# Kernel optimization log

Measured on AMD Instinct MI355X. Metric: run time of the kernel, lower is better.

## Reference

```python
import jax, jax.numpy as jnp
import numpy as np

B, C, W, H = 4, 64, 64, 64
CQK = C // 8  # query/key channels


def setup_inputs() -> dict:
    key = jax.random.key(0)
    ks = jax.random.split(key, 8)
    s = 0.05
    return {
        "x": jax.random.normal(ks[0], (B, C, W, H), jnp.float32),
        "Wq": jax.random.normal(ks[1], (CQK, C), jnp.float32) * s,
        "bq": jax.random.normal(ks[2], (CQK,), jnp.float32) * s,
        "Wk": jax.random.normal(ks[3], (CQK, C), jnp.float32) * s,
        "bk": jax.random.normal(ks[4], (CQK,), jnp.float32) * s,
        "Wv": jax.random.normal(ks[5], (C, C), jnp.float32) * s,
        "bv": jax.random.normal(ks[6], (C,), jnp.float32) * s,
        # torch init is zeros; use a nonzero value so the attention path is exercised
        "gamma": jax.random.normal(ks[7], (1,), jnp.float32) * s,
    }


def reference(x, Wq, bq, Wk, bk, Wv, bv, gamma):
    b, c, w, h = x.shape
    n = w * h
    xf = x.reshape(b, c, n)  # B, C, N
    # 1x1 convs == per-pixel linear maps
    q = jnp.einsum("oc,bcn->bno", Wq, xf) + bq           # B, N, Cqk
    k = jnp.einsum("oc,bcn->bon", Wk, xf) + bk[:, None]   # B, Cqk, N
    energy = jnp.einsum("bno,bom->bnm", q, k)             # B, N, N
    attn = jax.nn.softmax(energy, axis=-1)                # B, N, N
    v = jnp.einsum("oc,bcn->bon", Wv, xf) + bv[:, None]   # B, C, N
    # out[b,c,j] = sum_n v[b,c,n] * attn[j,n]  (bmm with attention^T)
    out = jnp.einsum("bcn,bjn->bcj", v, attn)
    out = out.reshape(b, c, w, h)
    return gamma * out + x
```

## Files before the change

### kernel.cpp

```cpp
#include <hip/hip_runtime.h>

typedef short s16x8 __attribute__((ext_vector_type(8)));
typedef float f32x4 __attribute__((ext_vector_type(4)));
typedef float f32x16 __attribute__((ext_vector_type(16)));
typedef unsigned u32x4 __attribute__((ext_vector_type(4)));

#define BB 4
#define NN 4096
#define LOG2E 1.4426950408889634f

__device__ __forceinline__ unsigned short f2bf(float f) {
    unsigned int u = __builtin_bit_cast(unsigned int, f);
    u += 0x7fff + ((u >> 16) & 1);
    return (unsigned short)(u >> 16);
}

__device__ __forceinline__ unsigned pk2(float lo, float hi) {
    return __builtin_amdgcn_perm(__builtin_bit_cast(unsigned, hi),
                                 __builtin_bit_cast(unsigned, lo), 0x07060302u);
}

__device__ __forceinline__ void gload16(const void* g, void* l) {
    __builtin_amdgcn_global_load_lds(
        (const __attribute__((address_space(1))) unsigned int*)g,
        (__attribute__((address_space(3))) unsigned int*)l, 16, 0, 0);
}

__device__ __forceinline__ void pl32swap(unsigned &a, unsigned &b) {
    asm volatile("v_permlane32_swap_b32 %0, %1" : "+v"(a), "+v"(b));
}

__global__ __launch_bounds__(256) void proj_kernel(
    const float* __restrict__ x,
    const float* __restrict__ Wq, const float* __restrict__ bq,
    const float* __restrict__ Wk, const float* __restrict__ bk,
    const float* __restrict__ Wv, const float* __restrict__ bv,
    unsigned short* __restrict__ Qw, unsigned short* __restrict__ Kw,
    unsigned short* __restrict__ Vw)
{
    __shared__ __attribute__((aligned(16))) unsigned short sW[80 * 72];
    __shared__ __attribute__((aligned(16))) unsigned short xT[64 * 72];
    __shared__ float sb[80];

    int tid = threadIdx.x;
    int b  = blockIdx.x >> 6;
    int n0 = (blockIdx.x & 63) << 6;

    for (int i = tid; i < 1280; i += 256) {
        int o = i >> 4, c4 = (i & 15) << 2;
        const float* src = (o < 8) ? &Wq[o * 64 + c4]
                         : ((o < 16) ? &Wk[(o - 8) * 64 + c4]
                                     : &Wv[(o - 16) * 64 + c4]);
        float4 v = *(const float4*)src;
        float sc = (o < 8) ? LOG2E : 1.f;
        sW[o * 72 + c4 + 0] = f2bf(v.x * sc);
        sW[o * 72 + c4 + 1] = f2bf(v.y * sc);
        sW[o * 72 + c4 + 2] = f2bf(v.z * sc);
        sW[o * 72 + c4 + 3] = f2bf(v.w * sc);
    }
    if (tid < 80)
        sb[tid] = (tid < 8) ? bq[tid] * LOG2E
                            : ((tid < 16) ? bk[tid - 8] : bv[tid - 16]);
    for (int i = tid; i < 1024; i += 256) {
        int c = i >> 4, p4 = (i & 15) << 2;
        float4 v = *(const float4*)&x[(((size_t)b * 64 + c) << 12) + n0 + p4];
        xT[(p4 + 0) * 72 + c] = f2bf(v.x);
        xT[(p4 + 1) * 72 + c] = f2bf(v.y);
        xT[(p4 + 2) * 72 + c] = f2bf(v.z);
        xT[(p4 + 3) * 72 + c] = f2bf(v.w);
    }
    __syncthreads();

    int w = tid >> 6, l = tid & 63, g = l >> 4, q16 = l & 15;
    int pix = w * 16 + q16;

    s16x8 bf0 = *(const s16x8*)&xT[pix * 72 + g * 8];
    s16x8 bf1 = *(const s16x8*)&xT[pix * 72 + 32 + g * 8];

    s16x8 a0[5], a1[5];
#pragma unroll
    for (int ot = 0; ot < 5; ++ot) {
        a0[ot] = *(const s16x8*)&sW[(ot * 16 + q16) * 72 + g * 8];
        a1[ot] = *(const s16x8*)&sW[(ot * 16 + q16) * 72 + 32 + g * 8];
    }
    __syncthreads();

    unsigned short* sV = xT;
    size_t base16 = ((size_t)(b << 12) + n0 + pix) << 4;

#pragma unroll
    for (int ot = 0; ot < 5; ++ot) {
        f32x4 acc = {0.f, 0.f, 0.f, 0.f};
        acc = __builtin_amdgcn_mfma_f32_16x16x32_bf16(a0[ot], bf0, acc, 0, 0, 0);
        acc = __builtin_amdgcn_mfma_f32_16x16x32_bf16(a1[ot], bf1, acc, 0, 0, 0);
#pragma unroll
        for (int r = 0; r < 4; ++r) {
            int orow = ot * 16 + g * 4 + r;
            unsigned short hv = f2bf(acc[r] + sb[orow]);
            if (ot == 0) {
                if (orow < 8) {
                    Qw[base16 + orow] = hv;
                    Qw[base16 + orow + 8] = 0;
                } else {
                    Kw[base16 + orow - 8] = hv;
                    Kw[base16 + orow] = 0;
                }
            } else {
                sV[(orow - 16) * 72 + pix] = hv;
            }
        }
    }
    __syncthreads();

#pragma unroll
    for (int i = tid; i < 512; i += 256) {
        int c = i >> 3, oct = i & 7;
        u32x4 v = *(const u32x4*)&sV[c * 72 + oct * 8];
        *(u32x4*)&Vw[(((size_t)b * 64 + c) << 12) + n0 + oct * 8] = v;
    }
}

__global__ __launch_bounds__(1024, 4) void attn_kernel(
    const unsigned short* __restrict__ Qw, const unsigned short* __restrict__ Kw,
    const unsigned short* __restrict__ Vw, const float* __restrict__ x,
    const float* __restrict__ gamma, float* __restrict__ out)
{
    __shared__ __attribute__((aligned(16))) char smem[150784];
    const int OOFF = 131072, LOFF = 148480, GLOFF = 150528;

    int tid = threadIdx.x;
    int w = tid >> 6, l = tid & 63, r31 = l & 31, hi = l >> 5;
    int wq = w >> 3, wk = w & 7;
    int b  = blockIdx.x >> 6;
    int n0 = (blockIdx.x & 63) << 6;
    float gm = gamma[0];

    const char* vsrc = (const char*)Vw + ((size_t)b << 19) + ((size_t)w << 13)
                     + ((l ^ (w & 7)) << 4);
    char* vdst = smem + w * 1024;

    const char* Qb = (const char*)Qw + ((size_t)b << 17);
    s16x8 qf = *(const s16x8*)(Qb + ((size_t)(n0 + wq * 32 + r31) << 5) + (hi << 4));
    const char* Kb = (const char*)Kw + ((size_t)b << 17)
                   + ((size_t)r31 << 5) + (hi << 4);

    f32x16 acc0, acc1;
#pragma unroll
    for (int i = 0; i < 16; ++i) { acc0[i] = 0.f; acc1[i] = 0.f; }
    float la = 0.f;

    gload16(vsrc, vdst);
    gload16(vsrc + (16 << 13), vdst + 16 * 1024);
    gload16(vsrc + (32 << 13), vdst + 32 * 1024);
    gload16(vsrc + (48 << 13), vdst + 48 * 1024);
    __syncthreads();

    for (int t = 0; t < 8; ++t) {
        int buf = t & 1;
        if (t < 7) {
            int bo = (buf ^ 1) << 16;
            const char* vs = vsrc + (size_t)(t + 1) * 1024;
            gload16(vs,             vdst + bo);
            gload16(vs + (16 << 13), vdst + bo + 16 * 1024);
            gload16(vs + (32 << 13), vdst + bo + 32 * 1024);
            gload16(vs + (48 << 13), vdst + bo + 48 * 1024);
        }
        const char* Vt = smem + (buf << 16);

        int kk0 = (t << 9) + (wk << 6);
        s16x8 kfA = *(const s16x8*)(Kb + ((size_t)kk0 << 5));
        s16x8 kfB = *(const s16x8*)(Kb + ((size_t)(kk0 + 32) << 5));

#pragma unroll
        for (int ci = 0; ci < 2; ++ci) {
            s16x8 kf = ci ? kfB : kfA;

            f32x16 E;
            {
                f32x16 z;
#pragma unroll
                for (int i = 0; i < 16; ++i) z[i] = 0.f;
                E = __builtin_amdgcn_mfma_f32_32x32x16_bf16(kf, qf, z, 0, 0, 0);
            }
#pragma unroll
            for (int i = 0; i < 16; ++i) E[i] = __builtin_amdgcn_exp2f(E[i]);
            la += (((E[0] + E[1]) + (E[2] + E[3])) + ((E[4] + E[5]) + (E[6] + E[7])))
                + (((E[8] + E[9]) + (E[10] + E[11])) + ((E[12] + E[13]) + (E[14] + E[15])));

            unsigned x0 = pk2(E[0], E[1]),  x1 = pk2(E[2], E[3]);
            unsigned x2 = pk2(E[4], E[5]),  x3 = pk2(E[6], E[7]);
            unsigned x4 = pk2(E[8], E[9]),  x5 = pk2(E[10], E[11]);
            unsigned x6 = pk2(E[12], E[13]), x7 = pk2(E[14], E[15]);
            pl32swap(x0, x2); pl32swap(x1, x3);
            pl32swap(x4, x6); pl32swap(x5, x7);
            u32x4 u0 = {x0, x1, x2, x3}, u1 = {x4, x5, x6, x7};
            s16x8 pf0 = __builtin_bit_cast(s16x8, u0);
            s16x8 pf1 = __builtin_bit_cast(s16x8, u1);

            int jb = (wk << 3) + (ci << 2);
            int sj0 = (((jb + hi) ^ (r31 & 7)) << 4);
            int sj1 = (((jb + 2 + hi) ^ (r31 & 7)) << 4);
            const char* row_lo = Vt + (r31 << 10);
            const char* row_hi = row_lo + (32 << 10);
            s16x8 vA0 = *(const s16x8*)(row_lo + sj0);
            s16x8 vA1 = *(const s16x8*)(row_lo + sj1);
            s16x8 vB0 = *(const s16x8*)(row_hi + sj0);
            s16x8 vB1 = *(const s16x8*)(row_hi + sj1);

            acc0 = __builtin_amdgcn_mfma_f32_32x32x16_bf16(vA0, pf0, acc0, 0, 0, 0);
            acc0 = __builtin_amdgcn_mfma_f32_32x32x16_bf16(vA1, pf1, acc0, 0, 0, 0);
            acc1 = __builtin_amdgcn_mfma_f32_32x32x16_bf16(vB0, pf0, acc1, 0, 0, 0);
            acc1 = __builtin_amdgcn_mfma_f32_32x32x16_bf16(vB1, pf1, acc1, 0, 0, 0);
        }
        __syncthreads();
    }

    la += __shfl_xor(la, 32);
    float* sL = (float*)(smem + LOFF);
    if (l < 32) sL[wk * 64 + wq * 32 + l] = la;

    float* sO = (float*)(smem + OOFF);
#pragma unroll
    for (int s = 0; s < 8; ++s) {
#pragma unroll
        for (int B = 0; B < 8; ++B) {
            if (((wk + s) & 7) == B) {
                const int R2 = B & 3;
                float e0 = (B < 4) ? acc0[R2 * 4 + 0] : acc1[R2 * 4 + 0];
                float e1 = (B < 4) ? acc0[R2 * 4 + 1] : acc1[R2 * 4 + 1];
                float e2 = (B < 4) ? acc0[R2 * 4 + 2] : acc1[R2 * 4 + 2];
                float e3 = (B < 4) ? acc0[R2 * 4 + 3] : acc1[R2 * 4 + 3];
                float* p = &sO[(B * 8 + hi * 4) * 68 + wq * 32 + r31];
                if (s == 0) {
                    p[0] = e0; p[68] = e1; p[136] = e2; p[204] = e3;
                } else {
                    p[0] += e0; p[68] += e1; p[136] += e2; p[204] += e3;
                }
            }
        }
        __syncthreads();
    }

    float* sGL = (float*)(smem + GLOFF);
    if (tid < 64) {
        float L = 0.f;
#pragma unroll
        for (int wk2 = 0; wk2 < 8; ++wk2) L += sL[wk2 * 64 + tid];
        sGL[tid] = gm / L;
    }
    __syncthreads();

#pragma unroll
    for (int pp = 0; pp < 4; ++pp) {
        int c = pp * 16 + w;
        size_t idx = (((size_t)b * 64 + c) << 12) + n0 + l;
        out[idx] = sGL[l] * sO[c * 68 + l] + x[idx];
    }
}

extern "C" void kernel_launch(void* const* d_in, const int* in_sizes, int n_in,
                              void* d_out, int out_size, void* d_ws, size_t ws_size,
                              hipStream_t stream) {
    const float* x     = (const float*)d_in[0];
    const float* Wq    = (const float*)d_in[1];
    const float* bq    = (const float*)d_in[2];
    const float* Wk    = (const float*)d_in[3];
    const float* bk    = (const float*)d_in[4];
    const float* Wv    = (const float*)d_in[5];
    const float* bv    = (const float*)d_in[6];
    const float* gamma = (const float*)d_in[7];
    float* out = (float*)d_out;

    unsigned short* Qw = (unsigned short*)d_ws;
    unsigned short* Kw = Qw + (size_t)BB * NN * 16;
    unsigned short* Vw = Kw + (size_t)BB * NN * 16;

    proj_kernel<<<256, 256, 0, stream>>>(x, Wq, bq, Wk, bk, Wv, bv, Qw, Kw, Vw);
    attn_kernel<<<256, 1024, 0, stream>>>(Qw, Kw, Vw, x, gamma, out);
}
```

Before: 31.51 us.

## Split attention into 512 blocks of 32 queries with 8 key-split waves

The attention kernel moves from 256 blocks of 1024 threads (64 queries, 2x8 waves) to 512 blocks of 512 threads (32 queries, 8 key-split waves). The halved shared-memory footprint allows two blocks per CU, and the K/V streaming loop now runs 16 smaller double-buffered steps, prefetching K fragments and waiting with vmcnt plus a raw barrier instead of a full syncthreads. The epilogue writes output with float4 vectorized stores. In exchange, V tiles are loaded twice as often across blocks and more barriers are executed per block.

Measured after the change: 34.82 us. +10.5%, slower.

```diff
diff --git a/kernel.cpp b/kernel.cpp
--- a/kernel.cpp
+++ b/kernel.cpp
@@ -120,141 +120,142 @@
     }
 }
 
-__global__ __launch_bounds__(1024, 4) void attn_kernel(
+__global__ __launch_bounds__(512, 2) void attn_kernel(
     const unsigned short* __restrict__ Qw, const unsigned short* __restrict__ Kw,
     const unsigned short* __restrict__ Vw, const float* __restrict__ x,
     const float* __restrict__ gamma, float* __restrict__ out)
 {
-    __shared__ __attribute__((aligned(16))) char smem[150784];
-    const int OOFF = 131072, LOFF = 148480, GLOFF = 150528;
+    __shared__ __attribute__((aligned(16))) char smem[75904];
+    const int OOFF = 65536, LOFF = 74752, GLOFF = 75776;
 
     int tid = threadIdx.x;
     int w = tid >> 6, l = tid & 63, r31 = l & 31, hi = l >> 5;
-    int wq = w >> 3, wk = w & 7;
-    int b  = blockIdx.x >> 6;
-    int n0 = (blockIdx.x & 63) << 6;
+    int b  = blockIdx.x >> 7;
+    int n0 = (blockIdx.x & 127) << 5;
     float gm = gamma[0];
 
-    const char* vsrc = (const char*)Vw + ((size_t)b << 19) + ((size_t)w << 13)
-                     + ((l ^ (w & 7)) << 4);
-    char* vdst = smem + w * 1024;
-
-    const char* Qb = (const char*)Qw + ((size_t)b << 17);
-    s16x8 qf = *(const s16x8*)(Qb + ((size_t)(n0 + wq * 32 + r31) << 5) + (hi << 4));
-    const char* Kb = (const char*)Kw + ((size_t)b << 17)
-                   + ((size_t)r31 << 5) + (hi << 4);
-
-    f32x16 acc0, acc1;
-#pragma unroll
-    for (int i = 0; i < 16; ++i) { acc0[i] = 0.f; acc1[i] = 0.f; }
+    const char* Vb = (const char*)Vw + ((size_t)b << 19);
+    const char* vs0, *vs1, *vs2, *vs3;
+    {
+        int rr = (w << 3) + hi;
+        vs0 = Vb + ((size_t)(rr + 0) << 13) + (((r31) ^ (0 + hi)) << 4);
+        vs1 = Vb + ((size_t)(rr + 2) << 13) + (((r31) ^ (2 + hi)) << 4);
+        vs2 = Vb + ((size_t)(rr + 4) << 13) + (((r31) ^ (4 + hi)) << 4);
+        vs3 = Vb + ((size_t)(rr + 6) << 13) + (((r31) ^ (6 + hi)) << 4);
+    }
+    char* vd = smem + (w << 12);
+
+    s16x8 qf = *(const s16x8*)((const char*)Qw + ((size_t)b << 17)
+                               + ((size_t)(n0 + r31) << 5) + (hi << 4));
+    const char* Kbw = (const char*)Kw + ((size_t)b << 17) + (w << 10)
+                    + ((size_t)r31 << 5) + (hi << 4);
+
+    f32x16 acc0, acc1, zz;
+#pragma unroll
+    for (int i = 0; i < 16; ++i) { acc0[i] = 0.f; acc1[i] = 0.f; zz[i] = 0.f; }
     float la = 0.f;
 
-    gload16(vsrc, vdst);
-    gload16(vsrc + (16 << 13), vdst + 16 * 1024);
-    gload16(vsrc + (32 << 13), vdst + 32 * 1024);
-    gload16(vsrc + (48 << 13), vdst + 48 * 1024);
-    __syncthreads();
-
-    for (int t = 0; t < 8; ++t) {
-        int buf = t & 1;
-        if (t < 7) {
-            int bo = (buf ^ 1) << 16;
-            const char* vs = vsrc + (size_t)(t + 1) * 1024;
-            gload16(vs,             vdst + bo);
-            gload16(vs + (16 << 13), vdst + bo + 16 * 1024);
-            gload16(vs + (32 << 13), vdst + bo + 32 * 1024);
-            gload16(vs + (48 << 13), vdst + bo + 48 * 1024);
-        }
-        const char* Vt = smem + (buf << 16);
-
-        int kk0 = (t << 9) + (wk << 6);
-        s16x8 kfA = *(const s16x8*)(Kb + ((size_t)kk0 << 5));
-        s16x8 kfB = *(const s16x8*)(Kb + ((size_t)(kk0 + 32) << 5));
-
-#pragma unroll
-        for (int ci = 0; ci < 2; ++ci) {
-            s16x8 kf = ci ? kfB : kfA;
-
-            f32x16 E;
-            {
-                f32x16 z;
-#pragma unroll
-                for (int i = 0; i < 16; ++i) z[i] = 0.f;
-                E = __builtin_amdgcn_mfma_f32_32x32x16_bf16(kf, qf, z, 0, 0, 0);
-            }
-#pragma unroll
-            for (int i = 0; i < 16; ++i) E[i] = __builtin_amdgcn_exp2f(E[i]);
-            la += (((E[0] + E[1]) + (E[2] + E[3])) + ((E[4] + E[5]) + (E[6] + E[7])))
-                + (((E[8] + E[9]) + (E[10] + E[11])) + ((E[12] + E[13]) + (E[14] + E[15])));
-
-            unsigned x0 = pk2(E[0], E[1]),  x1 = pk2(E[2], E[3]);
-            unsigned x2 = pk2(E[4], E[5]),  x3 = pk2(E[6], E[7]);
-            unsigned x4 = pk2(E[8], E[9]),  x5 = pk2(E[10], E[11]);
-            unsigned x6 = pk2(E[12], E[13]), x7 = pk2(E[14], E[15]);
-            pl32swap(x0, x2); pl32swap(x1, x3);
-            pl32swap(x4, x6); pl32swap(x5, x7);
-            u32x4 u0 = {x0, x1, x2, x3}, u1 = {x4, x5, x6, x7};
-            s16x8 pf0 = __builtin_bit_cast(s16x8, u0);
-            s16x8 pf1 = __builtin_bit_cast(s16x8, u1);
-
-            int jb = (wk << 3) + (ci << 2);
-            int sj0 = (((jb + hi) ^ (r31 & 7)) << 4);
-            int sj1 = (((jb + 2 + hi) ^ (r31 & 7)) << 4);
-            const char* row_lo = Vt + (r31 << 10);
-            const char* row_hi = row_lo + (32 << 10);
-            s16x8 vA0 = *(const s16x8*)(row_lo + sj0);
-            s16x8 vA1 = *(const s16x8*)(row_lo + sj1);
-            s16x8 vB0 = *(const s16x8*)(row_hi + sj0);
-            s16x8 vB1 = *(const s16x8*)(row_hi + sj1);
-
-            acc0 = __builtin_amdgcn_mfma_f32_32x32x16_bf16(vA0, pf0, acc0, 0, 0, 0);
-            acc0 = __builtin_amdgcn_mfma_f32_32x32x16_bf16(vA1, pf1, acc0, 0, 0, 0);
-            acc1 = __builtin_amdgcn_mfma_f32_32x32x16_bf16(vB0, pf0, acc1, 0, 0, 0);
-            acc1 = __builtin_amdgcn_mfma_f32_32x32x16_bf16(vB1, pf1, acc1, 0, 0, 0);
-        }
-        __syncthreads();
+    gload16(vs0, vd); gload16(vs1, vd + 1024);
+    gload16(vs2, vd + 2048); gload16(vs3, vd + 3072);
+    s16x8 kf_next = *(const s16x8*)(Kbw);
+    asm volatile("s_waitcnt vmcnt(1)" ::: "memory");
+    __builtin_amdgcn_s_barrier();
+
+    for (int t = 0; t < 16; ++t) {
+        s16x8 kf = kf_next;
+        const char* Vt = smem + ((t & 1) << 15);
+        if (t < 15) {
+            int bo = (((t & 1) ^ 1) << 15);
+            char* d = vd + bo;
+            size_t so = (size_t)(t + 1) << 9;
+            gload16(vs0 + so, d);        gload16(vs1 + so, d + 1024);
+            gload16(vs2 + so, d + 2048); gload16(vs3 + so, d + 3072);
+            kf_next = *(const s16x8*)(Kbw + ((size_t)(t + 1) << 13));
+        }
+
+        f32x16 E = __builtin_amdgcn_mfma_f32_32x32x16_bf16(kf, qf, zz, 0, 0, 0);
+#pragma unroll
+        for (int i = 0; i < 16; ++i) E[i] = __builtin_amdgcn_exp2f(E[i]);
+        la += (((E[0] + E[1]) + (E[2] + E[3])) + ((E[4] + E[5]) + (E[6] + E[7])))
+            + (((E[8] + E[9]) + (E[10] + E[11])) + ((E[12] + E[13]) + (E[14] + E[15])));
+
+        unsigned x0 = pk2(E[0], E[1]),   x1 = pk2(E[2], E[3]);
+        unsigned x2 = pk2(E[4], E[5]),   x3 = pk2(E[6], E[7]);
+        unsigned x4 = pk2(E[8], E[9]),   x5 = pk2(E[10], E[11]);
+        unsigned x6 = pk2(E[12], E[13]), x7 = pk2(E[14], E[15]);
+        pl32swap(x0, x2); pl32swap(x1, x3);
+        pl32swap(x4, x6); pl32swap(x5, x7);
+        u32x4 u0 = {x0, x1, x2, x3}, u1 = {x4, x5, x6, x7};
+        s16x8 pf0 = __builtin_bit_cast(s16x8, u0);
+        s16x8 pf1 = __builtin_bit_cast(s16x8, u1);
+
+        int sj0 = (((w << 2) + hi) ^ (r31 & 7)) << 4;
+        int sj1 = (((w << 2) + 2 + hi) ^ (r31 & 7)) << 4;
+        const char* row_lo = Vt + (r31 << 9);
+        const char* row_hi = row_lo + (32 << 9);
+        s16x8 vA0 = *(const s16x8*)(row_lo + sj0);
+        s16x8 vA1 = *(const s16x8*)(row_lo + sj1);
+        s16x8 vB0 = *(const s16x8*)(row_hi + sj0);
+        s16x8 vB1 = *(const s16x8*)(row_hi + sj1);
+
+        acc0 = __builtin_amdgcn_mfma_f32_32x32x16_bf16(vA0, pf0, acc0, 0, 0, 0);
+        acc0 = __builtin_amdgcn_mfma_f32_32x32x16_bf16(vA1, pf1, acc0, 0, 0, 0);
+        acc1 = __builtin_amdgcn_mfma_f32_32x32x16_bf16(vB0, pf0, acc1, 0, 0, 0);
+        acc1 = __builtin_amdgcn_mfma_f32_32x32x16_bf16(vB1, pf1, acc1, 0, 0, 0);
+
+        if (t < 15) {
+            asm volatile("s_waitcnt vmcnt(1)" ::: "memory");
+            __builtin_amdgcn_s_barrier();
+        }
     }
 
     la += __shfl_xor(la, 32);
     float* sL = (float*)(smem + LOFF);
-    if (l < 32) sL[wk * 64 + wq * 32 + l] = la;
+    if (l < 32) sL[w * 32 + l] = la;
 
     float* sO = (float*)(smem + OOFF);
 #pragma unroll
     for (int s = 0; s < 8; ++s) {
+        __syncthreads();
 #pragma unroll
         for (int B = 0; B < 8; ++B) {
-            if (((wk + s) & 7) == B) {
+            if (((w + s) & 7) == B) {
                 const int R2 = B & 3;
                 float e0 = (B < 4) ? acc0[R2 * 4 + 0] : acc1[R2 * 4 + 0];
                 float e1 = (B < 4) ? acc0[R2 * 4 + 1] : acc1[R2 * 4 + 1];
                 float e2 = (B < 4) ? acc0[R2 * 4 + 2] : acc1[R2 * 4 + 2];
                 float e3 = (B < 4) ? acc0[R2 * 4 + 3] : acc1[R2 * 4 + 3];
-                float* p = &sO[(B * 8 + hi * 4) * 68 + wq * 32 + r31];
+                float* p = &sO[(B * 8 + hi * 4) * 36 + r31];
                 if (s == 0) {
-                    p[0] = e0; p[68] = e1; p[136] = e2; p[204] = e3;
+                    p[0] = e0; p[36] = e1; p[72] = e2; p[108] = e3;
                 } else {
-                    p[0] += e0; p[68] += e1; p[136] += e2; p[204] += e3;
+                    p[0] += e0; p[36] += e1; p[72] += e2; p[108] += e3;
                 }
             }
         }
-        __syncthreads();
-    }
+    }
+    __syncthreads();
 
     float* sGL = (float*)(smem + GLOFF);
-    if (tid < 64) {
+    if (tid < 32) {
         float L = 0.f;
 #pragma unroll
-        for (int wk2 = 0; wk2 < 8; ++wk2) L += sL[wk2 * 64 + tid];
+        for (int wk2 = 0; wk2 < 8; ++wk2) L += sL[wk2 * 32 + tid];
         sGL[tid] = gm / L;
     }
     __syncthreads();
 
-#pragma unroll
-    for (int pp = 0; pp < 4; ++pp) {
-        int c = pp * 16 + w;
-        size_t idx = (((size_t)b * 64 + c) << 12) + n0 + l;
-        out[idx] = sGL[l] * sO[c * 68 + l] + x[idx];
+    {
+        int c = tid >> 3, qc = tid & 7;
+        float4 o4 = *(const float4*)&sO[c * 36 + qc * 4];
+        float4 g4 = *(const float4*)&sGL[qc * 4];
+        size_t idx = (((size_t)b * 64 + c) << 12) + n0 + qc * 4;
+        float4 x4v = *(const float4*)&x[idx];
+        o4.x = o4.x * g4.x + x4v.x;
+        o4.y = o4.y * g4.y + x4v.y;
+        o4.z = o4.z * g4.z + x4v.z;
+        o4.w = o4.w * g4.w + x4v.w;
+        *(float4*)&out[idx] = o4;
     }
 }
 
@@ -276,5 +277,5 @@
     unsigned short* Vw = Kw + (size_t)BB * NN * 16;
 
     proj_kernel<<<256, 256, 0, stream>>>(x, Wq, bq, Wk, bk, Wv, bv, Qw, Kw, Vw);
-    attn_kernel<<<256, 1024, 0, stream>>>(Qw, Kw, Vw, x, gamma, out);
-}
+    attn_kernel<<<512, 512, 0, stream>>>(Qw, Kw, Vw, x, gamma, out);
+}
```
